# Performance work log

Hardware: AMD Instinct MI355X
Metric: run time of the kernel (lower is better)

## Reference

```python
import jax, jax.numpy as jnp
import numpy as np

DIM = 2048
NH = 16
Q_LORA = 1536
KV_LORA = 512
NOPE = 128
ROPE = 64
VDIM = 128
QK = NOPE + ROPE  # 192
B, S = 2, 2048
EPS = 1.1920929e-07  # torch.finfo(float32).eps (nn.RMSNorm default)


def linear(x, w, b):
    return jnp.einsum('...i,oi->...o', x, w) + b


def rmsnorm(x, w):
    ms = jnp.mean(x * x, axis=-1, keepdims=True)
    return x * jax.lax.rsqrt(ms + EPS) * w


def rope(x, cos, sin):
    # x: [B,S,H,d] interleaved pairs; cos/sin: [S, d//2]
    x = x.reshape(*x.shape[:-1], -1, 2)
    x0, x1 = x[..., 0], x[..., 1]
    c = cos[None, :, None, :]
    s = sin[None, :, None, :]
    y0 = x0 * c - x1 * s
    y1 = x0 * s + x1 * c
    return jnp.stack([y0, y1], axis=-1).reshape(*x.shape[:-2], -1)


def setup_inputs() -> dict:
    key = jax.random.key(0)
    ks = jax.random.split(key, 12)
    sd = 0.02
    x = jax.random.normal(ks[0], (B, S, DIM), dtype=jnp.float32)
    freqs = jax.random.normal(ks[1], (S, ROPE // 2), dtype=jnp.float32)
    causal_mask = jnp.where(jnp.triu(jnp.ones((S, S), bool), k=1), -1e9, 0.0).astype(jnp.float32)
    inp = dict(x=x, freqs=freqs, causal_mask=causal_mask)
    inp['Wq_down_w'] = sd * jax.random.normal(ks[2], (Q_LORA, DIM), dtype=jnp.float32)
    inp['Wq_down_b'] = jnp.zeros((Q_LORA,), jnp.float32)
    inp['q_norm_w'] = jnp.ones((Q_LORA,), jnp.float32)
    inp['Wq_up_w'] = sd * jax.random.normal(ks[3], (NH * QK, Q_LORA), dtype=jnp.float32)
    inp['Wq_up_b'] = jnp.zeros((NH * QK,), jnp.float32)
    inp['Wkv_down_w'] = sd * jax.random.normal(ks[4], (KV_LORA + ROPE, DIM), dtype=jnp.float32)
    inp['Wkv_down_b'] = jnp.zeros((KV_LORA + ROPE,), jnp.float32)
    inp['kv_norm_w'] = jnp.ones((KV_LORA,), jnp.float32)
    inp['Wkv_up_w'] = sd * jax.random.normal(ks[5], (NH * (NOPE + VDIM), KV_LORA), dtype=jnp.float32)
    inp['Wkv_up_b'] = jnp.zeros((NH * (NOPE + VDIM),), jnp.float32)
    inp['Wo_w'] = sd * jax.random.normal(ks[6], (DIM, NH * VDIM), dtype=jnp.float32)
    inp['Wo_b'] = jnp.zeros((DIM,), jnp.float32)
    return inp


def reference(x, freqs, causal_mask, Wq_down_w, Wq_down_b, q_norm_w, Wq_up_w, Wq_up_b,
              Wkv_down_w, Wkv_down_b, kv_norm_w, Wkv_up_w, Wkv_up_b, Wo_w, Wo_b):
    cos, sin = jnp.cos(freqs), jnp.sin(freqs)
    scale = QK ** -0.5
    # Q path: low-rank down, RMSNorm, up
    q_lat = rmsnorm(linear(x, Wq_down_w, Wq_down_b), q_norm_w)
    Q = linear(q_lat, Wq_up_w, Wq_up_b).reshape(B, S, NH, QK)
    Q_nope, Q_rope = Q[..., :NOPE], Q[..., NOPE:]
    Q_rope = rope(Q_rope, cos, sin)
    Q = jnp.concatenate([Q_nope, Q_rope], axis=-1)  # [B,S,H,QK]
    # KV path: shared latent + decoupled rope key
    kv_kr = linear(x, Wkv_down_w, Wkv_down_b)
    kv_lat, K_rope = kv_kr[..., :KV_LORA], kv_kr[..., KV_LORA:]
    kv_lat = rmsnorm(kv_lat, kv_norm_w)
    K_rope = rope(K_rope[:, :, None, :], cos, sin)  # [B,S,1,ROPE]
    kv = linear(kv_lat, Wkv_up_w, Wkv_up_b).reshape(B, S, NH, NOPE + VDIM)
    K_nope, V = kv[..., :NOPE], kv[..., NOPE:]
    K = jnp.concatenate([K_nope, jnp.broadcast_to(K_rope, (B, S, NH, ROPE))], axis=-1)
    # attention
    scores = jnp.einsum('bqhd,bkhd->bhqk', Q, K) * scale + causal_mask[None, None]
    attn = jax.nn.softmax(scores, axis=-1)
    out = jnp.einsum('bhqk,bkhd->bqhd', attn, V).reshape(B, S, NH * VDIM)
    return linear(out, Wo_w, Wo_b)
```

## Files before the change

kernel.cpp:

```cpp
#include <hip/hip_runtime.h>
#include <hip/hip_bf16.h>

#define DIMD 2048
#define NHD 16
#define QLORA 1536
#define KVLORA 512
#define QKD 192
#define BBD 2
#define SSD 2048
#define BSD (BBD*SSD)
#define NDOWN 2176
#define BHN (BBD*NHD)
#define EPSF 1.1920929e-07f
#define SCALEF 0.07216878364870322f

typedef __hip_bfloat16 bf16;
typedef __attribute__((ext_vector_type(8))) short short8;
typedef __attribute__((ext_vector_type(4))) float floatx4;

typedef __attribute__((address_space(1))) char as1_char;
typedef __attribute__((address_space(3))) char as3_char;
#define GLD16(g, l) __builtin_amdgcn_global_load_lds((as1_char*)(g), (as3_char*)(l), 16, 0, 0)

__device__ __forceinline__ float block_sum(float x) {
#pragma unroll
  for (int o = 32; o > 0; o >>= 1) x += __shfl_xor(x, o, 64);
  __shared__ float red[4];
  __syncthreads();
  if ((threadIdx.x & 63) == 0) red[threadIdx.x >> 6] = x;
  __syncthreads();
  return red[0] + red[1] + red[2] + red[3];
}

template<bool STORE_BF16>
__global__ __launch_bounds__(256)
void gemm_bt(const bf16* __restrict__ A, const bf16* __restrict__ Bm,
             const float* __restrict__ bias, void* __restrict__ Cp,
             int M, int N, int K, long sA, long sB, long sC, int ldc)
{
  int nwg = gridDim.x * gridDim.y;
  int lin = blockIdx.y * gridDim.x + blockIdx.x;
  int xcd = lin & 7, l8 = lin >> 3;
  int qd = nwg >> 3, rd = nwg & 7;
  int wg = (xcd < rd ? xcd * (qd + 1) : rd * (qd + 1) + (xcd - rd) * qd) + l8;
  int bx = wg % gridDim.x, by = wg / gridDim.x;

  int m0 = by * 128, n0 = bx * 128;
  long z = blockIdx.z;
  A  += z * sA;
  Bm += z * sB;

  __shared__ __align__(16) bf16 Asm[128 * 64];
  __shared__ __align__(16) bf16 Bsm[128 * 64];

  const int tid  = threadIdx.x;
  const int lane = tid & 63;
  const int wv   = tid >> 6;
  const int wm   = (wv >> 1) << 6;
  const int wn   = (wv & 1) << 6;
  const int fr   = lane & 15;
  const int g4   = lane >> 4;

  int srow[4]; long sofs[4];
#pragma unroll
  for (int it = 0; it < 4; ++it) {
    int seg = it * 256 + tid;
    int row = seg >> 3, cs = seg & 7;
    srow[it] = row;
    sofs[it] = (long)row * 1 ;
    (void)cs;
  }
  int aoff[2][4], boff[2][4];
#pragma unroll
  for (int ks = 0; ks < 2; ++ks) {
#pragma unroll
    for (int t = 0; t < 4; ++t) {
      int ra = wm + t * 16 + fr;
      aoff[ks][t] = ra * 64 + (((ks * 4 + g4) ^ (ra & 7)) << 3);
      int rb = wn + t * 16 + fr;
      boff[ks][t] = rb * 64 + (((ks * 4 + g4) ^ (rb & 7)) << 3);
    }
  }

  floatx4 acc[4][4];
#pragma unroll
  for (int i = 0; i < 4; ++i)
#pragma unroll
    for (int j = 0; j < 4; ++j)
      acc[i][j] = (floatx4){0.f, 0.f, 0.f, 0.f};

  for (int k0 = 0; k0 < K; k0 += 64) {
    __syncthreads();
#pragma unroll
    for (int it = 0; it < 4; ++it) {
      int seg = it * 256 + tid;
      int row = seg >> 3, cs = seg & 7;
      int scs = cs ^ (row & 7);
      GLD16(A  + (long)(m0 + row) * K + k0 + scs * 8, &Asm[(it * 256 + wv * 64) * 8]);
      GLD16(Bm + (long)(n0 + row) * K + k0 + scs * 8, &Bsm[(it * 256 + wv * 64) * 8]);
    }
    __syncthreads();

#pragma unroll
    for (int ks = 0; ks < 2; ++ks) {
      short8 fa[4], fb[4];
#pragma unroll
      for (int t = 0; t < 4; ++t) fa[t] = *(const short8*)&Asm[aoff[ks][t]];
#pragma unroll
      for (int t = 0; t < 4; ++t) fb[t] = *(const short8*)&Bsm[boff[ks][t]];
      __builtin_amdgcn_s_setprio(1);
#pragma unroll
      for (int i = 0; i < 4; ++i)
#pragma unroll
        for (int j = 0; j < 4; ++j)
          acc[i][j] = __builtin_amdgcn_mfma_f32_16x16x32_bf16(fa[i], fb[j], acc[i][j], 0, 0, 0);
      __builtin_amdgcn_s_setprio(0);
    }
  }

  long cb = z * sC;
  int rq = g4 * 4;
#pragma unroll
  for (int i = 0; i < 4; ++i) {
#pragma unroll
    for (int j = 0; j < 4; ++j) {
      int col = n0 + wn + j * 16 + fr;
      float bv = bias ? bias[col] : 0.f;
#pragma unroll
      for (int r = 0; r < 4; ++r) {
        int rowg = m0 + wm + i * 16 + rq + r;
        float v = acc[i][j][r] + bv;
        if (STORE_BF16)
          ((bf16*)Cp)[cb + (long)rowg * ldc + col] = __float2bfloat16(v);
        else
          ((float*)Cp)[cb + (long)rowg * ldc + col] = v;
      }
    }
  }
}

__global__ __launch_bounds__(512, 2)
void flash_attn(const bf16* __restrict__ Qf, const bf16* __restrict__ Kh,
                const bf16* __restrict__ Vt, const float* __restrict__ freqs,
                bf16* __restrict__ attnall)
{
  const int lin = blockIdx.x;
  const int bh  = lin & 31;
  const int p   = lin >> 5;
  const int qtA = 15 - p;
  const int b = bh >> 4, h = bh & 15;

  const bf16* Qgf = Qf + (long)b * SSD * 3072 + h * QKD;
  const bf16* Kg  = Kh + (long)bh * SSD * QKD;
  const bf16* Vg  = Vt + (long)bh * 128 * SSD;

  __shared__ __align__(16) bf16 SM[57344];
  bf16* KB0 = SM;
  bf16* KB1 = SM + 12288;
  bf16* VB0 = SM + 24576;
  bf16* VB1 = SM + 32768;
  bf16* PB  = SM + 40960;

  const int tid  = threadIdx.x;
  const int lane = tid & 63;
  const int wv   = tid >> 6;
  const int w4   = wv & 3;
  const int tb   = wv >> 2;
  const int fr   = lane & 15;
  const int g4   = lane >> 4;

  const int qt    = tb ? (p) : (qtA);
  const int qbase = qt << 7;
  const int jmax  = 2 * qtA + 1;

  long kofs[3]; int kdst[3];
#pragma unroll
  for (int it = 0; it < 3; ++it) {
    int seg = it * 512 + tid;
    int c = seg >> 8, rs = seg & 255;
    int r = rs >> 2, s = (rs & 3) ^ ((r >> 1) & 3);
    kofs[it] = (long)r * QKD + c * 32 + s * 8;
    kdst[it] = c * 2048 + rs * 8;
  }
  long vofs[2]; int vdst[2];
#pragma unroll
  for (int it = 0; it < 2; ++it) {
    int seg = it * 512 + tid;
    int c2 = seg >> 9, ds = seg & 511;
    int d = ds >> 2, s = (ds & 3) ^ ((d >> 1) & 3);
    vofs[it] = (long)d * SSD + c2 * 32 + s * 8;
    vdst[it] = c2 * 4096 + ds * 8;
  }
  int fsw[4];
#pragma unroll
  for (int n = 0; n < 4; ++n) {
    int row = n * 16 + fr;
    fsw[n] = row * 32 + (((g4 ^ (row >> 1)) & 3) << 3);
  }
  int vsw[8];
#pragma unroll
  for (int dn = 0; dn < 8; ++dn) {
    int row = dn * 16 + fr;
    vsw[dn] = row * 32 + (((g4 ^ (row >> 1)) & 3) << 3);
  }
  int qoff[2];
#pragma unroll
  for (int i = 0; i < 2; ++i) {
    int row = wv * 32 + i * 16 + fr;
    qoff[i] = row * 32 + (((g4 ^ (row >> 1)) & 3) << 3);
  }

  const int qbA = qtA << 7, qbB = p << 7;
#pragma unroll
  for (int it = 0; it < 12; ++it) {
    int seg = it * 512 + tid;
    int c = seg >> 10, rs = seg & 1023;
    int r = rs >> 2, s = (rs & 3) ^ ((r >> 1) & 3);
    int tok = (r < 128) ? (qbA + r) : (qbB + r - 128);
    GLD16(Qgf + (long)tok * 3072 + c * 32 + s * 8, SM + c * 8192 + rs * 8);
  }
  __syncthreads();
  short8 qf[2][6];
#pragma unroll
  for (int i = 0; i < 2; ++i)
#pragma unroll
    for (int c = 0; c < 6; ++c)
      qf[i][c] = *(const short8*)(SM + c * 8192 + qoff[i]);

#pragma unroll
  for (int i = 0; i < 2; ++i) {
    int tok = qbase + w4 * 32 + i * 16 + fr;
    const float* fq = freqs + (long)tok * 32;
#pragma unroll
    for (int c = 0; c < 4; ++c) {
#pragma unroll
      for (int e = 0; e < 8; ++e) {
        bf16* el = (bf16*)&qf[i][c];
        el[e] = __float2bfloat16(__bfloat162float(el[e]) * SCALEF);
      }
    }
#pragma unroll
    for (int c = 4; c < 6; ++c) {
#pragma unroll
      for (int pp = 0; pp < 4; ++pp) {
        int jj = (c - 4) * 16 + g4 * 4 + pp;
        float f = fq[jj];
        float cs, sn;
        __sincosf(f, &sn, &cs);
        bf16* el = (bf16*)&qf[i][c];
        float x0 = __bfloat162float(el[2 * pp]);
        float x1 = __bfloat162float(el[2 * pp + 1]);
        el[2 * pp]     = __float2bfloat16((x0 * cs - x1 * sn) * SCALEF);
        el[2 * pp + 1] = __float2bfloat16((x0 * sn + x1 * cs) * SCALEF);
      }
    }
  }

  floatx4 oacc[2][8];
#pragma unroll
  for (int i = 0; i < 2; ++i)
#pragma unroll
    for (int n = 0; n < 8; ++n) oacc[i][n] = (floatx4){0.f, 0.f, 0.f, 0.f};
  float mi[2][4], li[2][4];
#pragma unroll
  for (int i = 0; i < 2; ++i)
#pragma unroll
    for (int r = 0; r < 4; ++r) { mi[i][r] = -1e30f; li[i][r] = 0.f; }

  __syncthreads();

  auto stageKV = [&](int jb2, bf16* kb2, bf16* vb2) {
#pragma unroll
    for (int it = 0; it < 3; ++it)
      GLD16(Kg + (long)jb2 * QKD + kofs[it], kb2 + kdst[it]);
#pragma unroll
    for (int it = 0; it < 2; ++it)
      GLD16(Vg + jb2 + vofs[it], vb2 + vdst[it]);
  };

  stageKV(0, KB0, VB0);

#pragma unroll 1
  for (int j = 0; j <= jmax; ++j) {
    const int jb = j << 6;
    if (j < jmax) {
      stageKV((j + 1) << 6, (j & 1) ? KB0 : KB1, (j & 1) ? VB0 : VB1);
      asm volatile("s_waitcnt vmcnt(5)" ::: "memory");
    } else {
      asm volatile("s_waitcnt vmcnt(0)" ::: "memory");
    }
    __builtin_amdgcn_sched_barrier(0);
    __builtin_amdgcn_s_barrier();
    __builtin_amdgcn_sched_barrier(0);

    const bf16* kb = (j & 1) ? KB1 : KB0;
    const bf16* vb = (j & 1) ? VB1 : VB0;
    const bool active = (jb <= qbase + w4 * 32 + 31);
    if (active) {
      floatx4 sacc[2][4];
#pragma unroll
      for (int i = 0; i < 2; ++i)
#pragma unroll
        for (int n = 0; n < 4; ++n) sacc[i][n] = (floatx4){0.f, 0.f, 0.f, 0.f};
      __builtin_amdgcn_s_setprio(1);
#pragma unroll
      for (int c = 0; c < 6; ++c) {
#pragma unroll
        for (int n = 0; n < 4; ++n) {
          short8 fb = *(const short8*)(kb + c * 2048 + fsw[n]);
#pragma unroll
          for (int i = 0; i < 2; ++i)
            sacc[i][n] = __builtin_amdgcn_mfma_f32_16x16x32_bf16(qf[i][c], fb, sacc[i][n], 0, 0, 0);
        }
      }
      __builtin_amdgcn_s_setprio(0);

      float pm[2][4];
#pragma unroll
      for (int i = 0; i < 2; ++i) {
        const int rbase = qbase + w4 * 32 + i * 16;
        const bool diag = (jb + 63 > rbase);
#pragma unroll
        for (int r = 0; r < 4; ++r) {
          if (diag) {
            int rowg = rbase + g4 * 4 + r;
#pragma unroll
            for (int n = 0; n < 4; ++n)
              if ((jb + n * 16 + fr) > rowg) sacc[i][n][r] = -1e30f;
          }
          pm[i][r] = fmaxf(fmaxf(sacc[i][0][r], sacc[i][1][r]),
                           fmaxf(sacc[i][2][r], sacc[i][3][r]));
        }
      }
      int nn = 0;
#pragma unroll
      for (int i = 0; i < 2; ++i)
#pragma unroll
        for (int r = 0; r < 4; ++r) nn |= (pm[i][r] > mi[i][r]);
      if (__any(nn)) {
#pragma unroll
        for (int i = 0; i < 2; ++i) {
#pragma unroll
          for (int r = 0; r < 4; ++r) {
            float mx = pm[i][r];
#pragma unroll
            for (int off = 1; off < 16; off <<= 1) mx = fmaxf(mx, __shfl_xor(mx, off, 64));
            float mnew = fmaxf(mi[i][r], mx);
            float alpha = __expf(mi[i][r] - mnew);
            mi[i][r] = mnew;
            li[i][r] *= alpha;
#pragma unroll
            for (int n = 0; n < 8; ++n) oacc[i][n][r] *= alpha;
          }
        }
      }
#pragma unroll
      for (int i = 0; i < 2; ++i) {
#pragma unroll
        for (int r = 0; r < 4; ++r) {
          float acc = 0.f;
#pragma unroll
          for (int n = 0; n < 4; ++n) {
            float pv = __expf(sacc[i][n][r] - mi[i][r]);
            sacc[i][n][r] = pv;
            acc += pv;
          }
          li[i][r] += acc;
        }
      }

#pragma unroll
      for (int i = 0; i < 2; ++i) {
#pragma unroll
        for (int n = 0; n < 4; ++n) {
          int c2 = n >> 1;
          int col = (n & 1) * 16 + fr;
#pragma unroll
          for (int r = 0; r < 4; ++r) {
            int m = wv * 32 + i * 16 + g4 * 4 + r;
            int cw = (((col >> 3) ^ ((m >> 1) & 3)) << 3) | (col & 7);
            PB[c2 * 8192 + m * 32 + cw] = __float2bfloat16(sacc[i][n][r]);
          }
        }
      }

      __builtin_amdgcn_s_setprio(1);
#pragma unroll
      for (int c2 = 0; c2 < 2; ++c2) {
        short8 pf[2];
#pragma unroll
        for (int i = 0; i < 2; ++i)
          pf[i] = *(const short8*)(PB + c2 * 8192 + qoff[i]);
#pragma unroll
        for (int dn = 0; dn < 8; ++dn) {
          short8 vf = *(const short8*)(vb + c2 * 4096 + vsw[dn]);
#pragma unroll
          for (int i = 0; i < 2; ++i)
            oacc[i][dn] = __builtin_amdgcn_mfma_f32_16x16x32_bf16(pf[i], vf, oacc[i][dn], 0, 0, 0);
        }
      }
      __builtin_amdgcn_s_setprio(0);
    }

    __builtin_amdgcn_sched_barrier(0);
    __builtin_amdgcn_s_barrier();
    __builtin_amdgcn_sched_barrier(0);
  }

#pragma unroll
  for (int i = 0; i < 2; ++i) {
#pragma unroll
    for (int r = 0; r < 4; ++r) {
      float l = li[i][r];
#pragma unroll
      for (int off = 1; off < 16; off <<= 1) l += __shfl_xor(l, off, 64);
      float inv = 1.f / l;
      int m = qbase + w4 * 32 + i * 16 + g4 * 4 + r;
      bf16* orow = attnall + ((long)(b * SSD + m) * NHD + h) * 128;
#pragma unroll
      for (int dn = 0; dn < 8; ++dn)
        orow[dn * 16 + fr] = __float2bfloat16(oacc[i][dn][r] * inv);
    }
  }
}

__device__ __forceinline__ void cvt4(const float* __restrict__ s, bf16* __restrict__ d,
                                     long se, long de) {
  float4 v = *(const float4*)(s + se);
  union { bf16 h[4]; uint2 u; } o;
  o.h[0] = __float2bfloat16(v.x); o.h[1] = __float2bfloat16(v.y);
  o.h[2] = __float2bfloat16(v.z); o.h[3] = __float2bfloat16(v.w);
  *(uint2*)(d + de) = o.u;
}

#define NX4   ((long)BSD * DIMD / 4)
#define NQD4  ((long)QLORA * DIMD / 4)
#define NKVD4 ((long)640 * DIMD / 4)
#define NQU4  ((long)3072 * QLORA / 4)
#define NKVU4 ((long)4096 * KVLORA / 4)
#define NWO4  ((long)DIMD * 2048 / 4)

__global__ __launch_bounds__(256)
void cvt_all(const float* __restrict__ x, const float* __restrict__ wqd,
             const float* __restrict__ wkvd, const float* __restrict__ wqu,
             const float* __restrict__ wkvu, const float* __restrict__ wo,
             bf16* __restrict__ dx, bf16* __restrict__ dwd, bf16* __restrict__ dwqu,
             bf16* __restrict__ dwkvu, bf16* __restrict__ dwo)
{
  long i = (long)blockIdx.x * 256 + threadIdx.x;
  if (i < NX4) { cvt4(x, dx, i * 4, i * 4); return; }
  i -= NX4;
  if (i < NQD4) { cvt4(wqd, dwd, i * 4, i * 4); return; }
  i -= NQD4;
  if (i < NKVD4) {
    long e = i * 4;
    long r = e >> 11;
    if (r < 576) cvt4(wkvd, dwd, e, (long)QLORA * DIMD + e);
    else *(uint2*)(dwd + (long)QLORA * DIMD + e) = (uint2){0u, 0u};
    return;
  }
  i -= NKVD4;
  if (i < NQU4) { cvt4(wqu, dwqu, i * 4, i * 4); return; }
  i -= NQU4;
  if (i < NKVU4) { cvt4(wkvu, dwkvu, i * 4, i * 4); return; }
  i -= NKVU4;
  if (i < NWO4) { cvt4(wo, dwo, i * 4, i * 4); return; }
}

template<int L>
__global__ __launch_bounds__(256)
void rmsnorm_k(const bf16* __restrict__ in, const float* __restrict__ bias,
               const float* __restrict__ w, bf16* __restrict__ out, int ldin)
{
  constexpr int NIT = L / 256;
  long r = blockIdx.x;
  const bf16* row = in + r * ldin;
  int tid = threadIdx.x;
  float v[NIT];
  float ss = 0.f;
#pragma unroll
  for (int i = 0; i < NIT; ++i) {
    int c = tid + (i << 8);
    float x = __bfloat162float(row[c]) + (bias ? bias[c] : 0.f);
    v[i] = x;
    ss += x * x;
  }
  ss = block_sum(ss);
  float sc = rsqrtf(ss / (float)L + EPSF);
#pragma unroll
  for (int i = 0; i < NIT; ++i) {
    int c = tid + (i << 8);
    out[r * L + c] = __float2bfloat16(v[i] * sc * w[c]);
  }
}

__global__ void build_k(const bf16* __restrict__ kvf, const bf16* __restrict__ kvkr,
                        const float* __restrict__ kvb, const float* __restrict__ freqs,
                        bf16* __restrict__ Kh)
{
  int idx = blockIdx.x * 256 + threadIdx.x;
  if (idx >= BSD * NHD * 96) return;
  int j = idx % 96;
  int h = (idx / 96) % NHD;
  int srow = idx / (96 * NHD);
  int s = srow & (SSD - 1);
  int b = srow >> 11;
  float y0, y1;
  if (j < 64) {
    const bf16* src = kvf + (long)srow * 4096 + h * 256 + 2 * j;
    y0 = __bfloat162float(src[0]); y1 = __bfloat162float(src[1]);
  } else {
    int i = j - 64;
    float x0 = __bfloat162float(kvkr[(long)srow * NDOWN + 512 + 2 * i]) + kvb[512 + 2 * i];
    float x1 = __bfloat162float(kvkr[(long)srow * NDOWN + 513 + 2 * i]) + kvb[513 + 2 * i];
    float f = freqs[s * 32 + i];
    float c, sn;
    __sincosf(f, &sn, &c);
    y0 = x0 * c - x1 * sn;
    y1 = x0 * sn + x1 * c;
  }
  bf16* dst = Kh + ((long)(b * NHD + h) * SSD + s) * QKD + 2 * j;
  dst[0] = __float2bfloat16(y0);
  dst[1] = __float2bfloat16(y1);
}

__global__ __launch_bounds__(256)
void build_vt(const bf16* __restrict__ kvf, bf16* __restrict__ Vt)
{
  __shared__ float t[32][33];
  int s0 = blockIdx.x * 32, d0 = blockIdx.y * 32, z = blockIdx.z;
  int b = z / NHD, h = z % NHD;
  int tx = threadIdx.x, ty = threadIdx.y;
#pragma unroll
  for (int r = 0; r < 4; ++r) {
    int sl = ty + r * 8;
    t[sl][tx] = __bfloat162float(kvf[(long)(b * SSD + s0 + sl) * 4096 + h * 256 + 128 + d0 + tx]);
  }
  __syncthreads();
#pragma unroll
  for (int r = 0; r < 4; ++r) {
    int dl = ty + r * 8;
    Vt[((long)z * 128 + d0 + dl) * SSD + s0 + tx] = __float2bfloat16(t[tx][dl]);
  }
}

__global__ void diag_fill(float* out) { out[blockIdx.x * 256 + threadIdx.x] = 1000.0f; }

extern "C" void kernel_launch(void* const* d_in, const int* in_sizes, int n_in,
                              void* d_out, int out_size, void* d_ws, size_t ws_size,
                              hipStream_t stream)
{
  const float* x     = (const float*)d_in[0];
  const float* freqs = (const float*)d_in[1];
  const float* Wqd   = (const float*)d_in[3];
  const float* Wqdb  = (const float*)d_in[4];
  const float* qnw   = (const float*)d_in[5];
  const float* Wqu   = (const float*)d_in[6];
  const float* Wqub  = (const float*)d_in[7];
  const float* Wkvd  = (const float*)d_in[8];
  const float* Wkvdb = (const float*)d_in[9];
  const float* kvnw  = (const float*)d_in[10];
  const float* Wkvu  = (const float*)d_in[11];
  const float* Wkvub = (const float*)d_in[12];
  const float* Wo    = (const float*)d_in[13];
  const float* Wob   = (const float*)d_in[14];
  float* out = (float*)d_out;

  char* ws = (char*)d_ws;
  size_t off = 0;
  auto alloc = [&](size_t bytes) {
    void* p = ws + off;
    off += (bytes + 255) & ~(size_t)255;
    return p;
  };

  bf16* Wd16   = (bf16*)alloc((size_t)NDOWN * DIMD * 2);
  bf16* Wqu16  = (bf16*)alloc((size_t)3072 * QLORA * 2);
  bf16* Wkvu16 = (bf16*)alloc((size_t)4096 * KVLORA * 2);
  bf16* Wo16   = (bf16*)alloc((size_t)DIMD * 2048 * 2);
  bf16* x16    = (bf16*)alloc((size_t)BSD * DIMD * 2);
  bf16* Ra     = (bf16*)alloc((size_t)BSD * NDOWN * 2);
  bf16* Rb     = (bf16*)alloc((size_t)BSD * QLORA * 2);
  bf16* Rc     = (bf16*)alloc((size_t)BSD * 4096 * 2);
  bf16* Qf     = (bf16*)alloc((size_t)BSD * 3072 * 2);
  bf16* Kh16   = (bf16*)alloc((size_t)BHN * SSD * QKD * 2);
  bf16* Vt16   = (bf16*)alloc((size_t)BHN * 128 * SSD * 2);

  bf16* qdown   = Ra;
  bf16* kvkr    = Ra + QLORA;
  bf16* qlat16  = Rb;  bf16* kvlat16 = Rb;
  bf16* kvf     = Rc;  bf16* attnall = Rc;

  if (off > ws_size) { diag_fill<<<8, 256, 0, stream>>>(out); return; }

  dim3 blk(256);
  auto cdiv = [](long a, long b) { return (int)((a + b - 1) / b); };

  long tot4 = NX4 + NQD4 + NKVD4 + NQU4 + NKVU4 + NWO4;
  cvt_all<<<cdiv(tot4, 256), blk, 0, stream>>>(x, Wqd, Wkvd, Wqu, Wkvu, Wo,
                                               x16, Wd16, Wqu16, Wkvu16, Wo16);

  gemm_bt<true><<<dim3(NDOWN / 128, BSD / 128, 1), blk, 0, stream>>>(
      x16, Wd16, nullptr, Ra, BSD, NDOWN, DIMD, 0, 0, 0, NDOWN);

  rmsnorm_k<QLORA><<<BSD, blk, 0, stream>>>(qdown, Wqdb, qnw, qlat16, NDOWN);
  gemm_bt<true><<<dim3(3072 / 128, BSD / 128, 1), blk, 0, stream>>>(
      qlat16, Wqu16, Wqub, Qf, BSD, 3072, QLORA, 0, 0, 0, 3072);

  rmsnorm_k<KVLORA><<<BSD, blk, 0, stream>>>(kvkr, Wkvdb, kvnw, kvlat16, NDOWN);
  gemm_bt<true><<<dim3(4096 / 128, BSD / 128, 1), blk, 0, stream>>>(
      kvlat16, Wkvu16, Wkvub, kvf, BSD, 4096, KVLORA, 0, 0, 0, 4096);
  build_k<<<cdiv((long)BSD * NHD * 96, 256), blk, 0, stream>>>(kvf, kvkr, Wkvdb, freqs, Kh16);
  build_vt<<<dim3(SSD / 32, 128 / 32, BHN), dim3(32, 8), 0, stream>>>(kvf, Vt16);

  flash_attn<<<dim3(256), dim3(512), 0, stream>>>(Qf, Kh16, Vt16, freqs, attnall);

  gemm_bt<false><<<dim3(2048 / 128, BSD / 128, 1), blk, 0, stream>>>(
      attnall, Wo16, Wob, out, BSD, DIMD, 2048, 0, 0, 0, DIMD);
}
```

Measured before the change: 469.2 us.

## Write Q and K_nope head-major from GEMM epilogues, double-buffer output projection GEMM

```diff
diff --git a/kernel.cpp b/kernel.cpp
--- a/kernel.cpp
+++ b/kernel.cpp
@@ -32,11 +32,11 @@
   return red[0] + red[1] + red[2] + red[3];
 }
 
-template<bool STORE_BF16>
+template<int MODE>
 __global__ __launch_bounds__(256)
 void gemm_bt(const bf16* __restrict__ A, const bf16* __restrict__ Bm,
              const float* __restrict__ bias, void* __restrict__ Cp,
-             int M, int N, int K, long sA, long sB, long sC, int ldc)
+             int K, int ldc, bf16* __restrict__ Kh)
 {
   int nwg = gridDim.x * gridDim.y;
   int lin = blockIdx.y * gridDim.x + blockIdx.x;
@@ -46,9 +46,6 @@
   int bx = wg % gridDim.x, by = wg / gridDim.x;
 
   int m0 = by * 128, n0 = bx * 128;
-  long z = blockIdx.z;
-  A  += z * sA;
-  Bm += z * sB;
 
   __shared__ __align__(16) bf16 Asm[128 * 64];
   __shared__ __align__(16) bf16 Bsm[128 * 64];
@@ -61,15 +58,6 @@
   const int fr   = lane & 15;
   const int g4   = lane >> 4;
 
-  int srow[4]; long sofs[4];
-#pragma unroll
-  for (int it = 0; it < 4; ++it) {
-    int seg = it * 256 + tid;
-    int row = seg >> 3, cs = seg & 7;
-    srow[it] = row;
-    sofs[it] = (long)row * 1 ;
-    (void)cs;
-  }
   int aoff[2][4], boff[2][4];
 #pragma unroll
   for (int ks = 0; ks < 2; ++ks) {
@@ -118,8 +106,9 @@
     }
   }
 
-  long cb = z * sC;
-  int rq = g4 * 4;
+  const int rq = g4 * 4;
+  const bool kvK = (MODE == 2) && ((n0 & 128) == 0);
+  const int kvh = n0 >> 8;
 #pragma unroll
   for (int i = 0; i < 4; ++i) {
 #pragma unroll
@@ -130,17 +119,139 @@
       for (int r = 0; r < 4; ++r) {
         int rowg = m0 + wm + i * 16 + rq + r;
         float v = acc[i][j][r] + bv;
-        if (STORE_BF16)
-          ((bf16*)Cp)[cb + (long)rowg * ldc + col] = __float2bfloat16(v);
-        else
-          ((float*)Cp)[cb + (long)rowg * ldc + col] = v;
+        if (MODE == 0) {
+          ((float*)Cp)[(long)rowg * ldc + col] = v;
+        } else if (MODE == 1) {
+          ((bf16*)Cp)[(long)rowg * ldc + col] = __float2bfloat16(v);
+        } else if (MODE == 2) {
+          if (kvK) {
+            int bb = rowg >> 11, s = rowg & (SSD - 1);
+            int jj = col & 255;
+            Kh[((long)(bb * NHD + kvh) * SSD + s) * QKD + jj] = __float2bfloat16(v);
+          } else {
+            ((bf16*)Cp)[(long)rowg * ldc + col] = __float2bfloat16(v);
+          }
+        } else {
+          unsigned h = (unsigned)col / 192u;
+          int jj = col - (int)h * 192;
+          int bb = rowg >> 11, s = rowg & (SSD - 1);
+          ((bf16*)Cp)[((long)(bb * NHD + (int)h) * SSD + s) * QKD + jj] = __float2bfloat16(v);
+        }
+      }
+    }
+  }
+}
+
+__global__ __launch_bounds__(256)
+void gemm_bt_db(const bf16* __restrict__ A, const bf16* __restrict__ Bm,
+                const float* __restrict__ bias, float* __restrict__ Cp, int K, int ldc)
+{
+  int nwg = gridDim.x * gridDim.y;
+  int lin = blockIdx.y * gridDim.x + blockIdx.x;
+  int xcd = lin & 7, l8 = lin >> 3;
+  int qd = nwg >> 3, rd = nwg & 7;
+  int wg = (xcd < rd ? xcd * (qd + 1) : rd * (qd + 1) + (xcd - rd) * qd) + l8;
+  int bx = wg % gridDim.x, by = wg / gridDim.x;
+  int m0 = by * 128, n0 = bx * 128;
+
+  __shared__ __align__(16) bf16 SA[2][8192];
+  __shared__ __align__(16) bf16 SB[2][8192];
+
+  const int tid  = threadIdx.x;
+  const int lane = tid & 63;
+  const int wv   = tid >> 6;
+  const int wm   = (wv >> 1) << 6;
+  const int wn   = (wv & 1) << 6;
+  const int fr   = lane & 15;
+  const int g4   = lane >> 4;
+
+  int aoff[2][4], boff[2][4];
+#pragma unroll
+  for (int ks = 0; ks < 2; ++ks) {
+#pragma unroll
+    for (int t = 0; t < 4; ++t) {
+      int ra = wm + t * 16 + fr;
+      aoff[ks][t] = ra * 64 + (((ks * 4 + g4) ^ (ra & 7)) << 3);
+      int rb = wn + t * 16 + fr;
+      boff[ks][t] = rb * 64 + (((ks * 4 + g4) ^ (rb & 7)) << 3);
+    }
+  }
+
+  floatx4 acc[4][4];
+#pragma unroll
+  for (int i = 0; i < 4; ++i)
+#pragma unroll
+    for (int j = 0; j < 4; ++j)
+      acc[i][j] = (floatx4){0.f, 0.f, 0.f, 0.f};
+
+  auto stage = [&](int t, int buf) {
+    const long k0 = (long)t << 6;
+#pragma unroll
+    for (int it = 0; it < 4; ++it) {
+      int seg = it * 256 + tid;
+      int row = seg >> 3, cs = seg & 7;
+      int scs = cs ^ (row & 7);
+      GLD16(A  + (long)(m0 + row) * K + k0 + scs * 8, &SA[buf][(it * 256 + wv * 64) * 8]);
+      GLD16(Bm + (long)(n0 + row) * K + k0 + scs * 8, &SB[buf][(it * 256 + wv * 64) * 8]);
+    }
+  };
+
+  const int nt = K >> 6;
+  stage(0, 0);
+
+#pragma unroll 1
+  for (int t = 0; t < nt; ++t) {
+    if (t + 1 < nt) {
+      stage(t + 1, (t + 1) & 1);
+      asm volatile("s_waitcnt vmcnt(8)" ::: "memory");
+    } else {
+      asm volatile("s_waitcnt vmcnt(0)" ::: "memory");
+    }
+    __builtin_amdgcn_sched_barrier(0);
+    __builtin_amdgcn_s_barrier();
+    __builtin_amdgcn_sched_barrier(0);
+
+    const bf16* abuf = SA[t & 1];
+    const bf16* bbuf = SB[t & 1];
+#pragma unroll
+    for (int ks = 0; ks < 2; ++ks) {
+      short8 fa[4], fb[4];
+#pragma unroll
+      for (int tt = 0; tt < 4; ++tt) fa[tt] = *(const short8*)(abuf + aoff[ks][tt]);
+#pragma unroll
+      for (int tt = 0; tt < 4; ++tt) fb[tt] = *(const short8*)(bbuf + boff[ks][tt]);
+      __builtin_amdgcn_s_setprio(1);
+#pragma unroll
+      for (int i = 0; i < 4; ++i)
+#pragma unroll
+        for (int j = 0; j < 4; ++j)
+          acc[i][j] = __builtin_amdgcn_mfma_f32_16x16x32_bf16(fa[i], fb[j], acc[i][j], 0, 0, 0);
+      __builtin_amdgcn_s_setprio(0);
+    }
+
+    __builtin_amdgcn_sched_barrier(0);
+    __builtin_amdgcn_s_barrier();
+    __builtin_amdgcn_sched_barrier(0);
+  }
+
+  int rq = g4 * 4;
+#pragma unroll
+  for (int i = 0; i < 4; ++i) {
+#pragma unroll
+    for (int j = 0; j < 4; ++j) {
+      int col = n0 + wn + j * 16 + fr;
+      float bv = bias ? bias[col] : 0.f;
+#pragma unroll
+      for (int r = 0; r < 4; ++r) {
+        int rowg = m0 + wm + i * 16 + rq + r;
+        Cp[(long)rowg * ldc + col] = acc[i][j][r] + bv;
       }
     }
   }
 }
 
 __global__ __launch_bounds__(512, 2)
-void flash_attn(const bf16* __restrict__ Qf, const bf16* __restrict__ Kh,
+void flash_attn(const bf16* __restrict__ Qh, const bf16* __restrict__ Kh,
                 const bf16* __restrict__ Vt, const float* __restrict__ freqs,
                 bf16* __restrict__ attnall)
 {
@@ -150,9 +261,9 @@
   const int qtA = 15 - p;
   const int b = bh >> 4, h = bh & 15;
 
-  const bf16* Qgf = Qf + (long)b * SSD * 3072 + h * QKD;
-  const bf16* Kg  = Kh + (long)bh * SSD * QKD;
-  const bf16* Vg  = Vt + (long)bh * 128 * SSD;
+  const bf16* Qg = Qh + (long)bh * SSD * QKD;
+  const bf16* Kg = Kh + (long)bh * SSD * QKD;
+  const bf16* Vg = Vt + (long)bh * 128 * SSD;
 
   __shared__ __align__(16) bf16 SM[57344];
   bf16* KB0 = SM;
@@ -173,6 +284,14 @@
   const int qbase = qt << 7;
   const int jmax  = 2 * qtA + 1;
 
+  float4 fq4[2][2];
+#pragma unroll
+  for (int i = 0; i < 2; ++i) {
+    int tok = qbase + w4 * 32 + i * 16 + fr;
+    fq4[i][0] = *(const float4*)(freqs + (long)tok * 32 + g4 * 4);
+    fq4[i][1] = *(const float4*)(freqs + (long)tok * 32 + 16 + g4 * 4);
+  }
+
   long kofs[3]; int kdst[3];
 #pragma unroll
   for (int it = 0; it < 3; ++it) {
@@ -217,7 +336,7 @@
     int c = seg >> 10, rs = seg & 1023;
     int r = rs >> 2, s = (rs & 3) ^ ((r >> 1) & 3);
     int tok = (r < 128) ? (qbA + r) : (qbB + r - 128);
-    GLD16(Qgf + (long)tok * 3072 + c * 32 + s * 8, SM + c * 8192 + rs * 8);
+    GLD16(Qg + (long)tok * QKD + c * 32 + s * 8, SM + c * 8192 + rs * 8);
   }
   __syncthreads();
   short8 qf[2][6];
@@ -227,10 +346,21 @@
     for (int c = 0; c < 6; ++c)
       qf[i][c] = *(const short8*)(SM + c * 8192 + qoff[i]);
 
+  __syncthreads();
+
+  auto stageKV = [&](int jb2, bf16* kb2, bf16* vb2) {
+#pragma unroll
+    for (int it = 0; it < 3; ++it)
+      GLD16(Kg + (long)jb2 * QKD + kofs[it], kb2 + kdst[it]);
+#pragma unroll
+    for (int it = 0; it < 2; ++it)
+      GLD16(Vg + jb2 + vofs[it], vb2 + vdst[it]);
+  };
+
+  stageKV(0, KB0, VB0);
+
 #pragma unroll
   for (int i = 0; i < 2; ++i) {
-    int tok = qbase + w4 * 32 + i * 16 + fr;
-    const float* fq = freqs + (long)tok * 32;
 #pragma unroll
     for (int c = 0; c < 4; ++c) {
 #pragma unroll
@@ -243,8 +373,7 @@
     for (int c = 4; c < 6; ++c) {
 #pragma unroll
       for (int pp = 0; pp < 4; ++pp) {
-        int jj = (c - 4) * 16 + g4 * 4 + pp;
-        float f = fq[jj];
+        float f = (c == 4) ? ((const float*)&fq4[i][0])[pp] : ((const float*)&fq4[i][1])[pp];
         float cs, sn;
         __sincosf(f, &sn, &cs);
         bf16* el = (bf16*)&qf[i][c];
@@ -266,19 +395,6 @@
   for (int i = 0; i < 2; ++i)
 #pragma unroll
     for (int r = 0; r < 4; ++r) { mi[i][r] = -1e30f; li[i][r] = 0.f; }
-
-  __syncthreads();
-
-  auto stageKV = [&](int jb2, bf16* kb2, bf16* vb2) {
-#pragma unroll
-    for (int it = 0; it < 3; ++it)
-      GLD16(Kg + (long)jb2 * QKD + kofs[it], kb2 + kdst[it]);
-#pragma unroll
-    for (int it = 0; it < 2; ++it)
-      GLD16(Vg + jb2 + vofs[it], vb2 + vdst[it]);
-  };
-
-  stageKV(0, KB0, VB0);
 
 #pragma unroll 1
   for (int j = 0; j <= jmax; ++j) {
@@ -494,34 +610,24 @@
   }
 }
 
-__global__ void build_k(const bf16* __restrict__ kvf, const bf16* __restrict__ kvkr,
-                        const float* __restrict__ kvb, const float* __restrict__ freqs,
-                        bf16* __restrict__ Kh)
+__global__ void build_k_rope(const bf16* __restrict__ kvkr, const float* __restrict__ kvb,
+                             const float* __restrict__ freqs, bf16* __restrict__ Kh)
 {
   int idx = blockIdx.x * 256 + threadIdx.x;
-  if (idx >= BSD * NHD * 96) return;
-  int j = idx % 96;
-  int h = (idx / 96) % NHD;
-  int srow = idx / (96 * NHD);
+  if (idx >= BSD * NHD * 32) return;
+  int i = idx & 31;
+  int h = (idx >> 5) & 15;
+  int srow = idx >> 9;
   int s = srow & (SSD - 1);
   int b = srow >> 11;
-  float y0, y1;
-  if (j < 64) {
-    const bf16* src = kvf + (long)srow * 4096 + h * 256 + 2 * j;
-    y0 = __bfloat162float(src[0]); y1 = __bfloat162float(src[1]);
-  } else {
-    int i = j - 64;
-    float x0 = __bfloat162float(kvkr[(long)srow * NDOWN + 512 + 2 * i]) + kvb[512 + 2 * i];
-    float x1 = __bfloat162float(kvkr[(long)srow * NDOWN + 513 + 2 * i]) + kvb[513 + 2 * i];
-    float f = freqs[s * 32 + i];
-    float c, sn;
-    __sincosf(f, &sn, &c);
-    y0 = x0 * c - x1 * sn;
-    y1 = x0 * sn + x1 * c;
-  }
-  bf16* dst = Kh + ((long)(b * NHD + h) * SSD + s) * QKD + 2 * j;
-  dst[0] = __float2bfloat16(y0);
-  dst[1] = __float2bfloat16(y1);
+  float x0 = __bfloat162float(kvkr[(long)srow * NDOWN + 512 + 2 * i]) + kvb[512 + 2 * i];
+  float x1 = __bfloat162float(kvkr[(long)srow * NDOWN + 513 + 2 * i]) + kvb[513 + 2 * i];
+  float f = freqs[s * 32 + i];
+  float c, sn;
+  __sincosf(f, &sn, &c);
+  bf16* dst = Kh + ((long)(b * NHD + h) * SSD + s) * QKD + 128 + 2 * i;
+  dst[0] = __float2bfloat16(x0 * c - x1 * sn);
+  dst[1] = __float2bfloat16(x0 * sn + x1 * c);
 }
 
 __global__ __launch_bounds__(256)
@@ -582,7 +688,7 @@
   bf16* Ra     = (bf16*)alloc((size_t)BSD * NDOWN * 2);
   bf16* Rb     = (bf16*)alloc((size_t)BSD * QLORA * 2);
   bf16* Rc     = (bf16*)alloc((size_t)BSD * 4096 * 2);
-  bf16* Qf     = (bf16*)alloc((size_t)BSD * 3072 * 2);
+  bf16* Qh16   = (bf16*)alloc((size_t)BHN * SSD * QKD * 2);
   bf16* Kh16   = (bf16*)alloc((size_t)BHN * SSD * QKD * 2);
   bf16* Vt16   = (bf16*)alloc((size_t)BHN * 128 * SSD * 2);
 
@@ -600,21 +706,21 @@
   cvt_all<<<cdiv(tot4, 256), blk, 0, stream>>>(x, Wqd, Wkvd, Wqu, Wkvu, Wo,
                                                x16, Wd16, Wqu16, Wkvu16, Wo16);
 
-  gemm_bt<true><<<dim3(NDOWN / 128, BSD / 128, 1), blk, 0, stream>>>(
-      x16, Wd16, nullptr, Ra, BSD, NDOWN, DIMD, 0, 0, 0, NDOWN);
+  gemm_bt<1><<<dim3(NDOWN / 128, BSD / 128), blk, 0, stream>>>(
+      x16, Wd16, nullptr, Ra, DIMD, NDOWN, nullptr);
 
   rmsnorm_k<QLORA><<<BSD, blk, 0, stream>>>(qdown, Wqdb, qnw, qlat16, NDOWN);
-  gemm_bt<true><<<dim3(3072 / 128, BSD / 128, 1), blk, 0, stream>>>(
-      qlat16, Wqu16, Wqub, Qf, BSD, 3072, QLORA, 0, 0, 0, 3072);
+  gemm_bt<3><<<dim3(3072 / 128, BSD / 128), blk, 0, stream>>>(
+      qlat16, Wqu16, Wqub, Qh16, QLORA, 3072, nullptr);
 
   rmsnorm_k<KVLORA><<<BSD, blk, 0, stream>>>(kvkr, Wkvdb, kvnw, kvlat16, NDOWN);
-  gemm_bt<true><<<dim3(4096 / 128, BSD / 128, 1), blk, 0, stream>>>(
-      kvlat16, Wkvu16, Wkvub, kvf, BSD, 4096, KVLORA, 0, 0, 0, 4096);
-  build_k<<<cdiv((long)BSD * NHD * 96, 256), blk, 0, stream>>>(kvf, kvkr, Wkvdb, freqs, Kh16);
+  gemm_bt<2><<<dim3(4096 / 128, BSD / 128), blk, 0, stream>>>(
+      kvlat16, Wkvu16, Wkvub, kvf, KVLORA, 4096, Kh16);
+  build_k_rope<<<cdiv((long)BSD * NHD * 32, 256), blk, 0, stream>>>(kvkr, Wkvdb, freqs, Kh16);
   build_vt<<<dim3(SSD / 32, 128 / 32, BHN), dim3(32, 8), 0, stream>>>(kvf, Vt16);
 
-  flash_attn<<<dim3(256), dim3(512), 0, stream>>>(Qf, Kh16, Vt16, freqs, attnall);
-
-  gemm_bt<false><<<dim3(2048 / 128, BSD / 128, 1), blk, 0, stream>>>(
-      attnall, Wo16, Wob, out, BSD, DIMD, 2048, 0, 0, 0, DIMD);
-}
+  flash_attn<<<dim3(256), dim3(512), 0, stream>>>(Qh16, Kh16, Vt16, freqs, attnall);
+
+  gemm_bt_db<<<dim3(2048 / 128, BSD / 128), blk, 0, stream>>>(
+      attnall, Wo16, Wob, out, 2048, DIMD);
+}
```

New measurement: 457.4 us. 2.5% less time.
